# Optimization experiments

Measured on AMD Instinct MI355X. Metric: run time of the kernel, lower is better.

## Reference

```python
import jax, jax.numpy as jnp
import numpy as np

EPS = 1e-8


def quaternion_mul(q, m):
    # Hamilton product q * m over last dim of size 4 (w, x, y, z)
    w1, x1, y1, z1 = q[..., 0], q[..., 1], q[..., 2], q[..., 3]
    w2, x2, y2, z2 = m[..., 0], m[..., 1], m[..., 2], m[..., 3]
    return jnp.stack([
        w1 * w2 - x1 * x2 - y1 * y2 - z1 * z2,
        w1 * x2 + x1 * w2 + y1 * z2 - z1 * y2,
        w1 * y2 - x1 * z2 + y1 * w2 + z1 * x2,
        w1 * z2 + x1 * y2 - y1 * x2 + z1 * w2,
    ], axis=-1)


def quaternion_normalize(q):
    n = jnp.linalg.norm(q, axis=-1, keepdims=True)
    return q / (n + EPS)


def setup_inputs() -> dict:
    key = jax.random.key(0)
    k = jax.random.split(key, 5)
    B, S, D, H = 4, 2048, 1024, 1024
    scale = 0.02
    return {
        "x": jax.random.normal(k[0], (B, S, D), dtype=jnp.float32),
        "W_in": jax.random.normal(k[1], (3 * H, D), dtype=jnp.float32) * scale,
        "b_in": jax.random.normal(k[2], (3 * H,), dtype=jnp.float32) * scale,
        "W_out": jax.random.normal(k[3], (D, 4 * H), dtype=jnp.float32) * scale,
        "b_out": jax.random.normal(k[4], (D,), dtype=jnp.float32) * scale,
    }


def reference(x, W_in, b_in, W_out, b_out):
    B, S, D = x.shape
    H = W_in.shape[0] // 3
    # input projection -> rotation parameters v in R^3 per hidden channel
    v = (jnp.einsum('bsd,ed->bse', x, W_in) + b_in).reshape(B, S, H, 3)
    # SU(2) exponential map: v -> unit quaternion
    theta = jnp.linalg.norm(v, axis=-1, keepdims=True)          # (B,S,H,1)
    axis = v / (theta + EPS)
    q_inputs = jnp.concatenate([jnp.cos(theta), jnp.sin(theta) * axis], axis=-1)  # (B,S,H,4)

    # initial identity quaternion state (B,H,4)
    m0 = jnp.zeros((B, H, 4), dtype=x.dtype).at[..., 0].set(1.0)

    def step(m, q_t):
        m_new = quaternion_normalize(quaternion_mul(q_t, m))
        return m_new, m_new

    q_seq = jnp.transpose(q_inputs, (1, 0, 2, 3))               # (S,B,H,4)
    m_final, ms = jax.lax.scan(step, m0, q_seq)                 # ms: (S,B,H,4)

    states = jnp.transpose(ms, (1, 0, 2, 3)).reshape(B, S, 4 * H)
    full_output = jnp.einsum('bsf,df->bsd', states, W_out) + b_out
    return full_output, m_final
```

## Files before the change

kernel.cpp:

```cpp
#include <hip/hip_runtime.h>
#include <hip/hip_bf16.h>
#include <stdint.h>

#define EPSF 1e-8f

typedef __attribute__((ext_vector_type(8))) short short8;
typedef __attribute__((ext_vector_type(8))) _Float16 half8;
typedef __attribute__((ext_vector_type(16))) float floatx16;

__device__ __forceinline__ unsigned short f2h(float f) {
    _Float16 h = (_Float16)f;
    return __builtin_bit_cast(unsigned short, h);
}
__device__ __forceinline__ float h2f(unsigned short u) {
    return (float)__builtin_bit_cast(_Float16, u);
}


__global__ void prep_kernel(const float4* __restrict__ x4, ushort4* __restrict__ x16,
                            const float4* __restrict__ wi4, ushort4* __restrict__ wi16,
                            const float4* __restrict__ wo4, ushort4* __restrict__ wo16,
                            int nx4, int nw4, int nwo4) {
    int i = blockIdx.x * blockDim.x + threadIdx.x;
    float4 f; ushort4 u;
    if (i < nx4) {
        f = x4[i];
        u.x = f2h(f.x); u.y = f2h(f.y); u.z = f2h(f.z); u.w = f2h(f.w);
        x16[i] = u;
    } else if (i < nx4 + nw4) {
        int j = i - nx4;
        f = wi4[j];
        u.x = f2h(f.x); u.y = f2h(f.y); u.z = f2h(f.z); u.w = f2h(f.w);
        wi16[j] = u;
    } else if (i < nx4 + nw4 + nwo4) {
        int j = i - nx4 - nw4;
        f = wo4[j];
        u.x = f2h(f.x); u.y = f2h(f.y); u.z = f2h(f.z); u.w = f2h(f.w);
        wo16[j] = u;
    }
}


__device__ __forceinline__ void gld16(const unsigned short* g, unsigned short* l) {
    __builtin_amdgcn_global_load_lds(
        (const __attribute__((address_space(1))) unsigned int*)g,
        (__attribute__((address_space(3))) unsigned int*)l, 16, 0, 0);
}

template <int BM, int BN, int BK, bool HALFOUT>
__global__ __launch_bounds__(256)
void gemm_bt(const unsigned short* __restrict__ Am, const unsigned short* __restrict__ Bm,
             const float* __restrict__ bias, void* __restrict__ Cv,
             int M, int N, int K) {
    constexpr int IF  = BM / 64;
    constexpr int JF  = BN / 64;
    constexpr int KH  = BK / 16;
    constexpr int CPR = BK / 8;
    extern __shared__ unsigned short smem[];
    unsigned short* sA = smem;
    unsigned short* sB = smem + BM * BK;

    const int tid  = threadIdx.x;
    const int lane = tid & 63;
    const int wid  = tid >> 6;
    const int wr   = wid >> 1, wc = wid & 1;
    const int m32  = lane & 31, half = lane >> 5;

    const int rowA0 = blockIdx.y * BM;
    const int rowB0 = blockIdx.x * BN;

    floatx16 acc[IF][JF];
#pragma unroll
    for (int i = 0; i < IF; i++)
#pragma unroll
        for (int j = 0; j < JF; j++)
#pragma unroll
            for (int r = 0; r < 16; r++) acc[i][j][r] = 0.f;

    const int nk = K / BK;
    for (int kt = 0; kt < nk; ++kt) {
        const int k0 = kt * BK;
#pragma unroll
        for (int i = 0; i < BM * CPR / 256; i++) {
            int c = tid + 256 * i;
            int r = c / CPR, ccl = c % CPR;
            int ccg = ccl ^ (r & (CPR - 1));
            gld16(Am + (size_t)(rowA0 + r) * K + k0 + ccg * 8, sA + c * 8);
        }
#pragma unroll
        for (int i = 0; i < BN * CPR / 256; i++) {
            int c = tid + 256 * i;
            int r = c / CPR, ccl = c % CPR;
            int ccg = ccl ^ (r & (CPR - 1));
            gld16(Bm + (size_t)(rowB0 + r) * K + k0 + ccg * 8, sB + c * 8);
        }
        __syncthreads();

#pragma unroll
        for (int kh = 0; kh < KH; kh++) {
            const int kc = kh * 2 + half;
            short8 a[IF], b[JF];
#pragma unroll
            for (int i = 0; i < IF; i++) {
                int ra = wr * (BM / 2) + i * 32 + m32;
                int pa = ra * CPR + (kc ^ (ra & (CPR - 1)));
                a[i] = *(const short8*)(sA + pa * 8);
            }
#pragma unroll
            for (int j = 0; j < JF; j++) {
                int rb = wc * (BN / 2) + j * 32 + m32;
                int pb = rb * CPR + (kc ^ (rb & (CPR - 1)));
                b[j] = *(const short8*)(sB + pb * 8);
            }
#pragma unroll
            for (int i = 0; i < IF; i++)
#pragma unroll
                for (int j = 0; j < JF; j++)
                    acc[i][j] = __builtin_amdgcn_mfma_f32_32x32x16_f16(
                        __builtin_bit_cast(half8, a[i]), __builtin_bit_cast(half8, b[j]),
                        acc[i][j], 0, 0, 0);
        }
        __syncthreads();
    }

#pragma unroll
    for (int i = 0; i < IF; i++) {
#pragma unroll
        for (int j = 0; j < JF; j++) {
            int col  = rowB0 + wc * (BN / 2) + j * 32 + m32;
            float bv = bias[col];
#pragma unroll
            for (int r = 0; r < 16; r++) {
                int row = rowA0 + wr * (BM / 2) + i * 32 + (r & 3) + 8 * (r >> 2) + 4 * half;
                if (HALFOUT)
                    ((unsigned short*)Cv)[(size_t)row * N + col] = f2h(acc[i][j][r] + bv);
                else
                    ((float*)Cv)[(size_t)row * N + col] = acc[i][j][r] + bv;
            }
        }
    }
}


struct Q { float w, x, y, z; };

__device__ __forceinline__ Q qmul(Q a, Q b) {
    Q r;
    r.w = a.w * b.w - a.x * b.x - a.y * b.y - a.z * b.z;
    r.x = a.w * b.x + a.x * b.w + a.y * b.z - a.z * b.y;
    r.y = a.w * b.y - a.x * b.z + a.y * b.w + a.z * b.x;
    r.z = a.w * b.z + a.x * b.y - a.y * b.x + a.z * b.w;
    return r;
}
__device__ __forceinline__ Q qnorm(Q a) {
    float nn = a.w * a.w + a.x * a.x + a.y * a.y + a.z * a.z;
    float inv = __frsqrt_rn(nn);
    Q r; r.w = a.w * inv; r.x = a.x * inv; r.y = a.y * inv; r.z = a.z * inv;
    return r;
}
__device__ __forceinline__ Q vquat(float vx, float vy, float vz) {
    float th = sqrtf(vx * vx + vy * vy + vz * vz);
    float s_, c_;
    __sincosf(th, &s_, &c_);
    float k = __fdividef(s_, th + EPSF);
    Q q; q.w = c_; q.x = k * vx; q.y = k * vy; q.z = k * vz;
    return q;
}

#define SEG  64
#define NSEG 32

__global__ __launch_bounds__(256)
void seg_prod_kernel(const unsigned short* __restrict__ v, float* __restrict__ partials,
                     int S, int H) {
    const int b  = blockIdx.z;
    const int h  = blockIdx.y * 64 + (threadIdx.x & 63);
    const int sg = blockIdx.x * 4 + (threadIdx.x >> 6);
    const int s0 = sg * SEG;
    const size_t vstep = (size_t)3 * H;
    const unsigned short* vp = v + ((size_t)b * S + s0) * vstep + (size_t)h * 3;

    constexpr int CH = 8;
    float ax[CH], ay[CH], az[CH], bx[CH], by[CH], bz[CH];
#pragma unroll
    for (int i = 0; i < CH; ++i) {
        ax[i] = h2f(vp[i * vstep + 0]); ay[i] = h2f(vp[i * vstep + 1]); az[i] = h2f(vp[i * vstep + 2]);
    }
    Q c = {1.f, 0.f, 0.f, 0.f};
    const int NC = SEG / CH;
    for (int cc = 0; cc < NC; cc += 2) {
        if (cc + 1 < NC) {
            const unsigned short* p = vp + (size_t)(cc + 1) * CH * vstep;
#pragma unroll
            for (int i = 0; i < CH; ++i) {
                bx[i] = h2f(p[i * vstep + 0]); by[i] = h2f(p[i * vstep + 1]); bz[i] = h2f(p[i * vstep + 2]);
            }
        }
#pragma unroll
        for (int i = 0; i < CH; ++i) c = qmul(vquat(ax[i], ay[i], az[i]), c);
        if (cc + 2 < NC) {
            const unsigned short* p = vp + (size_t)(cc + 2) * CH * vstep;
#pragma unroll
            for (int i = 0; i < CH; ++i) {
                ax[i] = h2f(p[i * vstep + 0]); ay[i] = h2f(p[i * vstep + 1]); az[i] = h2f(p[i * vstep + 2]);
            }
        }
#pragma unroll
        for (int i = 0; i < CH; ++i) c = qmul(vquat(bx[i], by[i], bz[i]), c);
    }
    float4* dst = (float4*)(partials + (((size_t)b * NSEG + sg) * H + h) * 4);
    *dst = make_float4(c.w, c.x, c.y, c.z);
}

__global__ __launch_bounds__(256)
void apply_kernel(const unsigned short* __restrict__ v, const float* __restrict__ partials,
                  unsigned short* __restrict__ st, float* __restrict__ m_final,
                  int S, int H) {
    const int b   = blockIdx.z;
    const int hb  = blockIdx.y * 64;
    const int hl  = threadIdx.x & 63;
    const int h   = hb + hl;
    const int sg  = blockIdx.x * 4 + (threadIdx.x >> 6);
    const int s0  = sg * SEG;
    const size_t vstep = (size_t)3 * H;
    const size_t sstep = (size_t)4 * H;
    const unsigned short* vp = v + ((size_t)b * S + s0) * vstep + (size_t)h * 3;
    unsigned short* sp = st + ((size_t)b * S + s0) * sstep + (size_t)h * 4;

    __shared__ float4 lp[NSEG][64];
    for (int i = threadIdx.x; i < NSEG * 64; i += 256) {
        int s2 = i >> 6, hh = i & 63;
        lp[s2][hh] = *(const float4*)(partials + (((size_t)b * NSEG + s2) * H + hb + hh) * 4);
    }
    __syncthreads();

    Q R = {1.f, 0.f, 0.f, 0.f};
    for (int s2 = 0; s2 < sg; ++s2) {
        float4 pv = lp[s2][hl];
        Q pq = {pv.x, pv.y, pv.z, pv.w};
        R = qmul(pq, R);
    }

    constexpr int CH = 8;
    float ax[CH], ay[CH], az[CH], bx[CH], by[CH], bz[CH];
#pragma unroll
    for (int i = 0; i < CH; ++i) {
        ax[i] = h2f(vp[i * vstep + 0]); ay[i] = h2f(vp[i * vstep + 1]); az[i] = h2f(vp[i * vstep + 2]);
    }
    const int NC = SEG / CH;
    for (int cc = 0; cc < NC; cc += 2) {
        if (cc + 1 < NC) {
            const unsigned short* pp = vp + (size_t)(cc + 1) * CH * vstep;
#pragma unroll
            for (int i = 0; i < CH; ++i) {
                bx[i] = h2f(pp[i * vstep + 0]); by[i] = h2f(pp[i * vstep + 1]); bz[i] = h2f(pp[i * vstep + 2]);
            }
        }
#pragma unroll
        for (int i = 0; i < CH; ++i) {
            R = qmul(vquat(ax[i], ay[i], az[i]), R);
            Q m = qnorm(R);
            ushort4 u; u.x = f2h(m.w); u.y = f2h(m.x); u.z = f2h(m.y); u.w = f2h(m.z);
            *(ushort4*)(sp + (size_t)(cc * CH + i) * sstep) = u;
        }
        if (cc + 2 < NC) {
            const unsigned short* pp = vp + (size_t)(cc + 2) * CH * vstep;
#pragma unroll
            for (int i = 0; i < CH; ++i) {
                ax[i] = h2f(pp[i * vstep + 0]); ay[i] = h2f(pp[i * vstep + 1]); az[i] = h2f(pp[i * vstep + 2]);
            }
        }
#pragma unroll
        for (int i = 0; i < CH; ++i) {
            R = qmul(vquat(bx[i], by[i], bz[i]), R);
            Q m = qnorm(R);
            ushort4 u; u.x = f2h(m.w); u.y = f2h(m.x); u.z = f2h(m.y); u.w = f2h(m.z);
            *(ushort4*)(sp + (size_t)((cc + 1) * CH + i) * sstep) = u;
        }
    }

    if (sg == NSEG - 1) {
        Q m = qnorm(R);
        float* mf = m_final + ((size_t)b * H + h) * 4;
        mf[0] = m.w; mf[1] = m.x; mf[2] = m.y; mf[3] = m.z;
    }
}


extern "C" void kernel_launch(void* const* d_in, const int* in_sizes, int n_in,
                              void* d_out, int out_size, void* d_ws, size_t ws_size,
                              hipStream_t stream) {
    const float* x     = (const float*)d_in[0];
    const float* W_in  = (const float*)d_in[1];
    const float* b_in  = (const float*)d_in[2];
    const float* W_out = (const float*)d_in[3];
    const float* b_out = (const float*)d_in[4];
    float* out = (float*)d_out;

    const int B = 4, S = 2048, D = 1024, H = 1024;
    const int M  = B * S;
    const int N1 = 3 * H;
    const int K1 = D;
    const int N2 = D;
    const int K2 = 4 * H;

    char* ws = (char*)d_ws;
    unsigned short* v    = (unsigned short*)(ws);
    unsigned short* st   = (unsigned short*)(ws + 50331648u);
    unsigned short* x16  = (unsigned short*)(ws + 50331648u);
    unsigned short* wi16 = (unsigned short*)(ws + 50331648u + 16777216u);
    unsigned short* wo16 = (unsigned short*)(ws + 117440512u);

    float* partials = out;

    const int nx  = M * K1;
    const int nw  = N1 * K1;
    const int nwo = N2 * K2;
    const int n4  = (nx + nw + nwo) / 4;

    prep_kernel<<<(n4 + 255) / 256, 256, 0, stream>>>(
        (const float4*)x, (ushort4*)x16, (const float4*)W_in, (ushort4*)wi16,
        (const float4*)W_out, (ushort4*)wo16, nx / 4, nw / 4, nwo / 4);

    gemm_bt<128, 128, 64, true><<<dim3(N1 / 128, M / 128), 256, 32768, stream>>>(
        x16, wi16, b_in, v, M, N1, K1);

    dim3 sg_grid(NSEG / 4, H / 64, B);
    seg_prod_kernel<<<sg_grid, 256, 0, stream>>>(v, partials, S, H);
    apply_kernel<<<sg_grid, 256, 0, stream>>>(v, partials, st, out + (size_t)M * D, S, H);

    gemm_bt<128, 128, 128, false><<<dim3(N2 / 128, M / 128), 256, 65536, stream>>>(
        st, wo16, b_out, out, M, N2, K2);
}
```

Baseline: 302.4 us.

## Replace GEMM with 8-wave triple-buffered pipelined kernel and XCD-aware tile swizzle

Swaps the simple single-buffered 128x128 GEMM for a 256x128-tile kernel with 512 threads. It triple-buffers LDS through direct global-to-LDS loads and prefetches two k-tiles ahead, using explicit vmcnt waits and barriers. Other changes are 16x16x32 MFMA, s_setprio around compute, and remapping block IDs across the 8 XCDs for L2 locality. The goal is to hide global load latency and raise MFMA utilisation in both projections. The cost is 144KB of LDS per block and a fragile hand-written wait and barrier schedule.

Measured after the change: 277.4 us. -8.3%, faster.

```diff
diff --git a/kernel.cpp b/kernel.cpp
--- a/kernel.cpp
+++ b/kernel.cpp
@@ -6,7 +6,7 @@
 
 typedef __attribute__((ext_vector_type(8))) short short8;
 typedef __attribute__((ext_vector_type(8))) _Float16 half8;
-typedef __attribute__((ext_vector_type(16))) float floatx16;
+typedef __attribute__((ext_vector_type(4))) float floatx4;
 
 __device__ __forceinline__ unsigned short f2h(float f) {
     _Float16 h = (_Float16)f;
@@ -47,95 +47,141 @@
         (__attribute__((address_space(3))) unsigned int*)l, 16, 0, 0);
 }
 
-template <int BM, int BN, int BK, bool HALFOUT>
-__global__ __launch_bounds__(256)
-void gemm_bt(const unsigned short* __restrict__ Am, const unsigned short* __restrict__ Bm,
-             const float* __restrict__ bias, void* __restrict__ Cv,
-             int M, int N, int K) {
-    constexpr int IF  = BM / 64;
-    constexpr int JF  = BN / 64;
-    constexpr int KH  = BK / 16;
-    constexpr int CPR = BK / 8;
+template <bool HALFOUT>
+__global__ __launch_bounds__(512, 2)
+void gemm8p(const unsigned short* __restrict__ Am, const unsigned short* __restrict__ Bm,
+            const float* __restrict__ bias, void* __restrict__ Cv,
+            int M, int N, int K) {
+    constexpr int BM = 256, BN = 128, BK = 64;
+    constexpr int ASZ  = BM * BK;
+    constexpr int BSZ  = BN * BK;
+    constexpr int SLOT = ASZ + BSZ;
     extern __shared__ unsigned short smem[];
-    unsigned short* sA = smem;
-    unsigned short* sB = smem + BM * BK;
 
     const int tid  = threadIdx.x;
     const int lane = tid & 63;
     const int wid  = tid >> 6;
-    const int wr   = wid >> 1, wc = wid & 1;
-    const int m32  = lane & 31, half = lane >> 5;
-
-    const int rowA0 = blockIdx.y * BM;
-    const int rowB0 = blockIdx.x * BN;
-
-    floatx16 acc[IF][JF];
-#pragma unroll
-    for (int i = 0; i < IF; i++)
-#pragma unroll
-        for (int j = 0; j < JF; j++)
-#pragma unroll
-            for (int r = 0; r < 16; r++) acc[i][j][r] = 0.f;
-
-    const int nk = K / BK;
-    for (int kt = 0; kt < nk; ++kt) {
-        const int k0 = kt * BK;
-#pragma unroll
-        for (int i = 0; i < BM * CPR / 256; i++) {
-            int c = tid + 256 * i;
-            int r = c / CPR, ccl = c % CPR;
-            int ccg = ccl ^ (r & (CPR - 1));
-            gld16(Am + (size_t)(rowA0 + r) * K + k0 + ccg * 8, sA + c * 8);
-        }
-#pragma unroll
-        for (int i = 0; i < BN * CPR / 256; i++) {
-            int c = tid + 256 * i;
-            int r = c / CPR, ccl = c % CPR;
-            int ccg = ccl ^ (r & (CPR - 1));
-            gld16(Bm + (size_t)(rowB0 + r) * K + k0 + ccg * 8, sB + c * 8);
-        }
-        __syncthreads();
-
-#pragma unroll
-        for (int kh = 0; kh < KH; kh++) {
-            const int kc = kh * 2 + half;
-            short8 a[IF], b[JF];
-#pragma unroll
-            for (int i = 0; i < IF; i++) {
-                int ra = wr * (BM / 2) + i * 32 + m32;
-                int pa = ra * CPR + (kc ^ (ra & (CPR - 1)));
-                a[i] = *(const short8*)(sA + pa * 8);
-            }
-#pragma unroll
-            for (int j = 0; j < JF; j++) {
-                int rb = wc * (BN / 2) + j * 32 + m32;
-                int pb = rb * CPR + (kc ^ (rb & (CPR - 1)));
-                b[j] = *(const short8*)(sB + pb * 8);
-            }
-#pragma unroll
-            for (int i = 0; i < IF; i++)
-#pragma unroll
-                for (int j = 0; j < JF; j++)
-                    acc[i][j] = __builtin_amdgcn_mfma_f32_32x32x16_f16(
-                        __builtin_bit_cast(half8, a[i]), __builtin_bit_cast(half8, b[j]),
-                        acc[i][j], 0, 0, 0);
-        }
-        __syncthreads();
-    }
-
-#pragma unroll
-    for (int i = 0; i < IF; i++) {
-#pragma unroll
-        for (int j = 0; j < JF; j++) {
-            int col  = rowB0 + wc * (BN / 2) + j * 32 + m32;
-            float bv = bias[col];
-#pragma unroll
-            for (int r = 0; r < 16; r++) {
-                int row = rowA0 + wr * (BM / 2) + i * 32 + (r & 3) + 8 * (r >> 2) + 4 * half;
+    const int wr   = wid >> 1;
+    const int wc   = wid & 1;
+    const int q4   = lane >> 4;
+    const int m16  = lane & 15;
+    const int x7   = m16 & 7;
+
+    const int nbx = N / BN;
+    const int nwg = gridDim.x;
+    const int q   = nwg >> 3;
+    const int wg  = blockIdx.x;
+    const int sz  = (wg & 7) * q + (wg >> 3);
+    const int bx  = sz % nbx, by = sz / nbx;
+    const int rowA0 = by * BM, rowB0 = bx * BN;
+
+    const int rA = tid >> 3, cA = tid & 7;
+    const int cg = cA ^ (rA & 7);
+    const unsigned short* srcA = Am + (size_t)(rowA0 + rA) * K + cg * 8;
+    const unsigned short* srcB = Bm + (size_t)(rowB0 + rA) * K + cg * 8;
+    const int dA = tid * 8;
+
+    int aoffm[4], boffn[4];
+#pragma unroll
+    for (int m = 0; m < 4; ++m) aoffm[m] = (wr * 64 + m * 16 + m16) * BK;
+#pragma unroll
+    for (int n = 0; n < 4; ++n) boffn[n] = (wc * 64 + n * 16 + m16) * BK;
+
+    floatx4 acc[4][4];
+#pragma unroll
+    for (int m = 0; m < 4; ++m)
+#pragma unroll
+        for (int n = 0; n < 4; ++n)
+#pragma unroll
+            for (int r = 0; r < 4; ++r) acc[m][n][r] = 0.f;
+
+    const int NT = K / BK;
+
+    auto stageA = [&](int s, int t, int j) {
+        gld16(srcA + (size_t)(j * 64) * K + (size_t)t * BK,
+              smem + s * SLOT + j * 4096 + dA);
+    };
+    auto stageB = [&](int s, int t, int j) {
+        gld16(srcB + (size_t)(j * 64) * K + (size_t)t * BK,
+              smem + s * SLOT + ASZ + j * 4096 + dA);
+    };
+
+#pragma unroll
+    for (int j = 0; j < 4; ++j) stageA(0, 0, j);
+    stageB(0, 0, 0); stageB(0, 0, 1);
+#pragma unroll
+    for (int j = 0; j < 4; ++j) stageA(1, 1, j);
+    stageB(1, 1, 0); stageB(1, 1, 1);
+
+    int s0 = 0;
+    for (int t = 0; t < NT; ++t) {
+        int s2 = s0 + 2; if (s2 >= 3) s2 -= 3;
+        if (t + 1 < NT) asm volatile("s_waitcnt vmcnt(6)" ::: "memory");
+        else            asm volatile("s_waitcnt vmcnt(0)" ::: "memory");
+        __builtin_amdgcn_s_barrier();
+        __builtin_amdgcn_sched_barrier(0);
+
+        const unsigned short* tA = smem + s0 * SLOT;
+        const unsigned short* tB = tA + ASZ;
+        const bool pf = (t + 2 < NT);
+
+        short8 av[4], bv[4];
+
+        {
+            const int xo = ((0 + q4) ^ x7) * 8;
+#pragma unroll
+            for (int m = 0; m < 4; ++m) av[m] = *(const short8*)(tA + aoffm[m] + xo);
+#pragma unroll
+            for (int n = 0; n < 4; ++n) bv[n] = *(const short8*)(tB + boffn[n] + xo);
+        }
+        if (pf) { stageA(s2, t + 2, 0); stageA(s2, t + 2, 1); stageB(s2, t + 2, 0); }
+        __builtin_amdgcn_s_barrier();
+        __builtin_amdgcn_s_setprio(1);
+#pragma unroll
+        for (int m = 0; m < 4; ++m)
+#pragma unroll
+            for (int n = 0; n < 4; ++n)
+                acc[m][n] = __builtin_amdgcn_mfma_f32_16x16x32_f16(
+                    __builtin_bit_cast(half8, av[m]), __builtin_bit_cast(half8, bv[n]),
+                    acc[m][n], 0, 0, 0);
+        __builtin_amdgcn_s_setprio(0);
+        __builtin_amdgcn_s_barrier();
+
+        {
+            const int xo = ((4 + q4) ^ x7) * 8;
+#pragma unroll
+            for (int m = 0; m < 4; ++m) av[m] = *(const short8*)(tA + aoffm[m] + xo);
+#pragma unroll
+            for (int n = 0; n < 4; ++n) bv[n] = *(const short8*)(tB + boffn[n] + xo);
+        }
+        if (pf) { stageA(s2, t + 2, 2); stageA(s2, t + 2, 3); stageB(s2, t + 2, 1); }
+        __builtin_amdgcn_s_barrier();
+        __builtin_amdgcn_s_setprio(1);
+#pragma unroll
+        for (int m = 0; m < 4; ++m)
+#pragma unroll
+            for (int n = 0; n < 4; ++n)
+                acc[m][n] = __builtin_amdgcn_mfma_f32_16x16x32_f16(
+                    __builtin_bit_cast(half8, av[m]), __builtin_bit_cast(half8, bv[n]),
+                    acc[m][n], 0, 0, 0);
+        __builtin_amdgcn_s_setprio(0);
+
+        s0 = (s0 + 1 == 3) ? 0 : s0 + 1;
+    }
+
+#pragma unroll
+    for (int m = 0; m < 4; ++m) {
+#pragma unroll
+        for (int n = 0; n < 4; ++n) {
+            int col  = rowB0 + wc * 64 + n * 16 + m16;
+            float bvl = bias[col];
+#pragma unroll
+            for (int r = 0; r < 4; ++r) {
+                int row = rowA0 + wr * 64 + m * 16 + q4 * 4 + r;
                 if (HALFOUT)
-                    ((unsigned short*)Cv)[(size_t)row * N + col] = f2h(acc[i][j][r] + bv);
+                    ((unsigned short*)Cv)[(size_t)row * N + col] = f2h(acc[m][n][r] + bvl);
                 else
-                    ((float*)Cv)[(size_t)row * N + col] = acc[i][j][r] + bv;
+                    ((float*)Cv)[(size_t)row * N + col] = acc[m][n][r] + bvl;
             }
         }
     }
@@ -318,17 +364,27 @@
     const int nwo = N2 * K2;
     const int n4  = (nx + nw + nwo) / 4;
 
+    constexpr int LDSB = 147456;
+    static int attr_done = 0;
+    if (!attr_done) {
+        hipFuncSetAttribute(reinterpret_cast<const void*>(&gemm8p<true>),
+                            hipFuncAttributeMaxDynamicSharedMemorySize, LDSB);
+        hipFuncSetAttribute(reinterpret_cast<const void*>(&gemm8p<false>),
+                            hipFuncAttributeMaxDynamicSharedMemorySize, LDSB);
+        attr_done = 1;
+    }
+
     prep_kernel<<<(n4 + 255) / 256, 256, 0, stream>>>(
         (const float4*)x, (ushort4*)x16, (const float4*)W_in, (ushort4*)wi16,
         (const float4*)W_out, (ushort4*)wo16, nx / 4, nw / 4, nwo / 4);
 
-    gemm_bt<128, 128, 64, true><<<dim3(N1 / 128, M / 128), 256, 32768, stream>>>(
+    gemm8p<true><<<dim3((M / 256) * (N1 / 128)), 512, LDSB, stream>>>(
         x16, wi16, b_in, v, M, N1, K1);
 
     dim3 sg_grid(NSEG / 4, H / 64, B);
     seg_prod_kernel<<<sg_grid, 256, 0, stream>>>(v, partials, S, H);
     apply_kernel<<<sg_grid, 256, 0, stream>>>(v, partials, st, out + (size_t)M * D, S, H);
 
-    gemm_bt<128, 128, 128, false><<<dim3(N2 / 128, M / 128), 256, 65536, stream>>>(
+    gemm8p<false><<<dim3((M / 256) * (N2 / 128)), 512, LDSB, stream>>>(
         st, wo16, b_out, out, M, N2, K2);
 }
```
